# Optimization experiments

Hardware: AMD Instinct MI355X
Metric: run time of the kernel (lower is better)

Reference implementation:

```python
import jax, jax.numpy as jnp
import numpy as np

N, E, F_IN, C, H, G = 50000, 800000, 128, 64, 4, 512

def _gat_layer(x, src, dst, W, a_src, a_dst, b):
    # x: [N, Fin]; W: [Fin, H*C]; a_src/a_dst: [H, C]; b: [C]
    n = x.shape[0]
    h = (x @ W).reshape(n, H, C)                      # [N,H,C]
    al_s = jnp.einsum('nhc,hc->nh', h, a_src)         # [N,H]
    al_d = jnp.einsum('nhc,hc->nh', h, a_dst)
    alpha = jax.nn.leaky_relu(al_s[src] + al_d[dst], 0.2)   # [Et,H]
    m = jax.ops.segment_max(alpha, dst, num_segments=n)      # segment softmax over dst
    e = jnp.exp(alpha - m[dst])
    s = jax.ops.segment_sum(e, dst, num_segments=n)
    coef = e / (s[dst] + 1e-16)                        # [Et,H]
    msg = h[src] * coef[:, :, None]                    # [Et,H,C]
    out = jax.ops.segment_sum(msg, dst, num_segments=n)
    return out.mean(axis=1) + b                        # concat=False: average heads

def setup_inputs():
    key = jax.random.key(0)
    ks = jax.random.split(key, 24)
    x = jax.random.normal(ks[0], (N, F_IN), jnp.float32)
    edge_index = jax.random.randint(ks[1], (2, E), 0, N, jnp.int64)
    edge_attr = jax.random.normal(ks[2], (E, 4), jnp.float32)
    batch_index = jnp.sort(jax.random.randint(ks[3], (N,), 0, G, jnp.int64))
    p = lambda k, shp: jax.random.normal(k, shp, jnp.float32) * 0.05
    inp = {
        'x': x, 'edge_index': edge_index, 'edge_attr': edge_attr, 'batch_index': batch_index,
        'W0': p(ks[4], (F_IN, H * C)), 'as0': p(ks[5], (H, C)), 'ad0': p(ks[6], (H, C)), 'b0': jnp.zeros((C,), jnp.float32),
        'W1': p(ks[7], (C, H * C)), 'as1': p(ks[8], (H, C)), 'ad1': p(ks[9], (H, C)), 'b1': jnp.zeros((C,), jnp.float32),
        'W2': p(ks[10], (C, H * C)), 'as2': p(ks[11], (H, C)), 'ad2': p(ks[12], (H, C)), 'b2': jnp.zeros((C,), jnp.float32),
        'Wr1': p(ks[13], (2 * C, C)), 'br1': jnp.zeros((C,), jnp.float32),
        'Wr2': p(ks[14], (C, 1)), 'br2': jnp.zeros((1,), jnp.float32),
    }
    return inp

def reference(x, edge_index, edge_attr, batch_index,
              W0, as0, ad0, b0, W1, as1, ad1, b1, W2, as2, ad2, b2,
              Wr1, br1, Wr2, br2):
    # add self-loops (PyG GATConv default add_self_loops=True); edge_attr unused (edge_dim=None)
    loop = jnp.arange(N, dtype=edge_index.dtype)
    src = jnp.concatenate([edge_index[0], loop])
    dst = jnp.concatenate([edge_index[1], loop])
    h = jax.nn.leaky_relu(_gat_layer(x, src, dst, W0, as0, ad0, b0))
    h = jax.nn.leaky_relu(_gat_layer(h, src, dst, W1, as1, ad1, b1))
    h = jax.nn.leaky_relu(_gat_layer(h, src, dst, W2, as2, ad2, b2))
    gmp = jax.ops.segment_max(h, batch_index, num_segments=G)           # [G,C]
    cnt = jax.ops.segment_sum(jnp.ones((N,), h.dtype), batch_index, num_segments=G)
    gap = jax.ops.segment_sum(h, batch_index, num_segments=G) / jnp.maximum(cnt, 1.0)[:, None]
    hid = jnp.concatenate([gmp, gap], axis=1)                            # [G,2C]
    hid = jax.nn.leaky_relu(hid @ Wr1 + br1)
    return hid @ Wr2 + br2                                               # [G,1]
```

## Files before the change

### kernel.cpp

```cpp
#include <hip/hip_runtime.h>
#include <hip/hip_bf16.h>
#include <hip/hip_fp16.h>

#define NN   50000
#define EE   800000
#define FIN  128
#define CC   64
#define HH   4
#define GG   512
#define CAP  64

__device__ __forceinline__ float leaky02(float x) { return x >= 0.f ? x : 0.2f * x; }
__device__ __forceinline__ float leaky01(float x) { return x >= 0.f ? x : 0.01f * x; }

__global__ __launch_bounds__(256) void build_csr(const int* __restrict__ ei,
                                                 int* __restrict__ deg,
                                                 int* __restrict__ csr) {
    int e = blockIdx.x * 256 + threadIdx.x;
    if (e >= EE) return;
    int s = ei[e];
    int d = ei[EE + e];
    if ((unsigned)d >= NN || (unsigned)s >= NN) return;
    int pos = atomicAdd(&deg[d], 1);
    if (pos < CAP) csr[d * CAP + pos] = s;
}

template <int K>
__global__ __launch_bounds__(256, 3) void gemm_gat(const float* __restrict__ x,
                                                   const float* __restrict__ W,
                                                   const float* __restrict__ a_src,
                                                   const float* __restrict__ a_dst,
                                                   __half* __restrict__ h_out,
                                                   float* __restrict__ al_s,
                                                   float* __restrict__ al_d) {
    __shared__ float Xs[32 * 128];
    __shared__ float Ws[32 * 128];
    const int t  = threadIdx.x;
    const int tc = t & 15;
    const int tr = t >> 4;
    const int r0 = blockIdx.x * 128;
    const int c0 = blockIdx.y * 128;

    float acc[8][8];
#pragma unroll
    for (int i = 0; i < 8; ++i)
#pragma unroll
        for (int j = 0; j < 8; ++j) acc[i][j] = 0.f;

    for (int k0 = 0; k0 < K; k0 += 32) {
#pragma unroll
        for (int jj = 0; jj < 4; ++jj) {
            int id = t + jj * 256;
            int m  = id >> 3;
            int k4 = id & 7;
            int row = r0 + m;
            row = row < NN ? row : NN - 1;
            float4 v = *(const float4*)(x + (size_t)row * K + k0 + k4 * 4);
#pragma unroll
            for (int c = 0; c < 4; ++c) {
                int k = k4 * 4 + c;
                int slot = (m >> 3) ^ (k >> 2);
                Xs[k * 128 + slot * 8 + (m & 7)] = ((const float*)&v)[c];
            }
        }
#pragma unroll
        for (int jj = 0; jj < 4; ++jj) {
            int id = t + jj * 256;
            int k  = id >> 5;
            int n4 = id & 31;
            float4 v = *(const float4*)(W + (size_t)(k0 + k) * 256 + c0 + n4 * 4);
            *(float4*)(Ws + k * 128 + n4 * 4) = v;
        }
        __syncthreads();

#pragma unroll
        for (int k = 0; k < 32; ++k) {
            int aslot = tr ^ (k >> 2);
            const float* ax = &Xs[k * 128 + aslot * 8];
            const float* bw = &Ws[k * 128 + tc * 8];
            float a0[8], b0[8];
            *(float4*)&a0[0] = *(const float4*)&ax[0];
            *(float4*)&a0[4] = *(const float4*)&ax[4];
            *(float4*)&b0[0] = *(const float4*)&bw[0];
            *(float4*)&b0[4] = *(const float4*)&bw[4];
#pragma unroll
            for (int i = 0; i < 8; ++i)
#pragma unroll
                for (int j = 0; j < 8; ++j)
                    acc[i][j] = fmaf(a0[i], b0[j], acc[i][j]);
        }
        __syncthreads();
    }

    const int colbase = c0 + tc * 8;
    const int head = colbase >> 6;
    float as_c[8], ad_c[8];
#pragma unroll
    for (int j = 0; j < 8; ++j) {
        as_c[j] = a_src[colbase + j];
        ad_c[j] = a_dst[colbase + j];
    }
#pragma unroll
    for (int i = 0; i < 8; ++i) {
        int row = r0 + tr * 8 + i;
        bool ok = row < NN;
        if (ok) {
            __half2 p0 = __floats2half2_rn(acc[i][0], acc[i][1]);
            __half2 p1 = __floats2half2_rn(acc[i][2], acc[i][3]);
            __half2 p2 = __floats2half2_rn(acc[i][4], acc[i][5]);
            __half2 p3 = __floats2half2_rn(acc[i][6], acc[i][7]);
            uint4 pk;
            pk.x = *(unsigned int*)&p0;
            pk.y = *(unsigned int*)&p1;
            pk.z = *(unsigned int*)&p2;
            pk.w = *(unsigned int*)&p3;
            *(uint4*)(h_out + (size_t)row * 256 + colbase) = pk;
        }
        float ps = 0.f, pd = 0.f;
#pragma unroll
        for (int j = 0; j < 8; ++j) {
            ps = fmaf(acc[i][j], as_c[j], ps);
            pd = fmaf(acc[i][j], ad_c[j], pd);
        }
#pragma unroll
        for (int off = 1; off <= 4; off <<= 1) {
            ps += __shfl_xor(ps, off, 64);
            pd += __shfl_xor(pd, off, 64);
        }
        if (ok && (tc & 7) == 0) {
            al_s[(size_t)row * 4 + head] = ps;
            al_d[(size_t)row * 4 + head] = pd;
        }
    }
}

struct Half8 { __half2 h[4]; };

__global__ __launch_bounds__(256) void gat_aggregate(const __half* __restrict__ h_buf,
                                                     const float* __restrict__ al_s,
                                                     const float* __restrict__ al_d,
                                                     const int* __restrict__ deg,
                                                     const int* __restrict__ csr,
                                                     const float* __restrict__ bias,
                                                     float* __restrict__ xout) {
    __shared__ __align__(16) __half2 els[4][66][4];
    const int w    = threadIdx.x >> 6;
    const int lane = threadIdx.x & 63;
    const int n    = blockIdx.x * 4 + w;
    const int d = min(deg[n], CAP);

    float4 ad4 = *(const float4*)(al_d + (size_t)n * 4);
    float4 as4 = *(const float4*)(al_s + (size_t)n * 4);
    const float* adp = (const float*)&ad4;
    const float* asp = (const float*)&as4;

    float aself[4];
#pragma unroll
    for (int h = 0; h < 4; ++h) aself[h] = leaky02(asp[h] + adp[h]);

    int s_lane = 0;
    float a_lane[4];
    if (lane < d) {
        s_lane = csr[(size_t)n * CAP + lane];
        float4 s4 = *(const float4*)(al_s + (size_t)s_lane * 4);
        const float* sp = (const float*)&s4;
#pragma unroll
        for (int h = 0; h < 4; ++h) a_lane[h] = leaky02(sp[h] + adp[h]);
    } else {
#pragma unroll
        for (int h = 0; h < 4; ++h) a_lane[h] = -INFINITY;
    }

    float mx[4];
#pragma unroll
    for (int h = 0; h < 4; ++h) {
        mx[h] = fmaxf(aself[h], a_lane[h]);
#pragma unroll
        for (int off = 32; off; off >>= 1) mx[h] = fmaxf(mx[h], __shfl_xor(mx[h], off, 64));
    }

    float e[4], sm[4];
#pragma unroll
    for (int h = 0; h < 4; ++h) {
        e[h] = (lane < d) ? expf(a_lane[h] - mx[h]) : 0.f;
        sm[h] = e[h];
#pragma unroll
        for (int off = 32; off; off >>= 1) sm[h] += __shfl_xor(sm[h], off, 64);
    }
    float eself[4], inv[4];
#pragma unroll
    for (int h = 0; h < 4; ++h) {
        eself[h] = expf(aself[h] - mx[h]);
        inv[h] = 1.f / (sm[h] + eself[h] + 1e-16f);
    }
    if (lane < d) {
#pragma unroll
        for (int h = 0; h < 4; ++h) {
            float c = e[h] * inv[h];
            els[w][lane + 1][h] = __floats2half2_rn(c, c);
        }
    }
    if (lane == 0) {
#pragma unroll
        for (int h = 0; h < 4; ++h) {
            float c = eself[h] * inv[h];
            els[w][0][h] = __floats2half2_rn(c, c);
        }
    }

    const int q    = lane >> 5;
    const int m    = lane & 31;
    const int head = m >> 3;
    const __half* __restrict__ hb = h_buf + m * 8;

    __half2 z = __floats2half2_rn(0.f, 0.f);
    __half2 acc0 = z, acc1 = z, acc2 = z, acc3 = z;
    const int count = d + 1;
    for (int t2 = 0; 2 * t2 < count; ++t2) {
        int v = 2 * t2 + q;
        int vi = v > 0 ? v - 1 : 0;
        int s = __shfl(s_lane, vi, 64);
        s = v == 0 ? n : s;
        if (v < count) {
            __half2 c2 = els[w][v][head];
            Half8 r = *(const Half8*)(hb + (size_t)s * 256);
            acc0 = __hfma2(r.h[0], c2, acc0);
            acc1 = __hfma2(r.h[1], c2, acc1);
            acc2 = __hfma2(r.h[2], c2, acc2);
            acc3 = __hfma2(r.h[3], c2, acc3);
        }
    }

    int i0 = __shfl_xor(*(int*)&acc0, 32, 64);
    int i1 = __shfl_xor(*(int*)&acc1, 32, 64);
    int i2 = __shfl_xor(*(int*)&acc2, 32, 64);
    int i3 = __shfl_xor(*(int*)&acc3, 32, 64);
    acc0 = __hadd2(acc0, *(__half2*)&i0);
    acc1 = __hadd2(acc1, *(__half2*)&i1);
    acc2 = __hadd2(acc2, *(__half2*)&i2);
    acc3 = __hadd2(acc3, *(__half2*)&i3);

    float ch[8];
    float2 f;
    f = __half22float2(acc0); ch[0] = f.x; ch[1] = f.y;
    f = __half22float2(acc1); ch[2] = f.x; ch[3] = f.y;
    f = __half22float2(acc2); ch[4] = f.x; ch[5] = f.y;
    f = __half22float2(acc3); ch[6] = f.x; ch[7] = f.y;
#pragma unroll
    for (int k = 0; k < 8; ++k) {
        ch[k] += __shfl_xor(ch[k], 8, 64);
        ch[k] += __shfl_xor(ch[k], 16, 64);
    }
    if (lane < 8) {
        float4 o0, o1;
        o0.x = leaky01(ch[0] * 0.25f + bias[lane * 8 + 0]);
        o0.y = leaky01(ch[1] * 0.25f + bias[lane * 8 + 1]);
        o0.z = leaky01(ch[2] * 0.25f + bias[lane * 8 + 2]);
        o0.w = leaky01(ch[3] * 0.25f + bias[lane * 8 + 3]);
        o1.x = leaky01(ch[4] * 0.25f + bias[lane * 8 + 4]);
        o1.y = leaky01(ch[5] * 0.25f + bias[lane * 8 + 5]);
        o1.z = leaky01(ch[6] * 0.25f + bias[lane * 8 + 6]);
        o1.w = leaky01(ch[7] * 0.25f + bias[lane * 8 + 7]);
        *(float4*)(xout + (size_t)n * 64 + lane * 8)     = o0;
        *(float4*)(xout + (size_t)n * 64 + lane * 8 + 4) = o1;
    }
}

__global__ __launch_bounds__(256) void readout(const float* __restrict__ x,
                                               const int* __restrict__ batch,
                                               float* __restrict__ gmp,
                                               float* __restrict__ gap) {
    int g = blockIdx.x;
    int a = 0, b = NN;
    while (a < b) { int m = (a + b) >> 1; if (batch[m] < g) a = m + 1; else b = m; }
    int lo = a;
    a = lo; b = NN;
    while (a < b) { int m = (a + b) >> 1; if (batch[m] < g + 1) a = m + 1; else b = m; }
    int hi = a;

    int t = threadIdx.x, c = t & 63, s = t >> 6;
    float mx = -INFINITY, sm = 0.f;
    for (int n = lo + s; n < hi; n += 4) {
        float v = x[(size_t)n * 64 + c];
        mx = fmaxf(mx, v);
        sm += v;
    }
    __shared__ float smx[256], ssm[256];
    smx[t] = mx; ssm[t] = sm;
    __syncthreads();
    if (t < 64) {
        mx = fmaxf(fmaxf(smx[t], smx[t + 64]), fmaxf(smx[t + 128], smx[t + 192]));
        sm = ssm[t] + ssm[t + 64] + ssm[t + 128] + ssm[t + 192];
        int cnt = hi - lo;
        gmp[g * 64 + t] = mx;
        gap[g * 64 + t] = sm / fmaxf((float)cnt, 1.0f);
    }
}

__global__ __launch_bounds__(64) void mlp_readout(const float* __restrict__ gmp,
                                                  const float* __restrict__ gap,
                                                  const float* __restrict__ Wr1,
                                                  const float* __restrict__ br1,
                                                  const float* __restrict__ Wr2,
                                                  const float* __restrict__ br2,
                                                  float* __restrict__ out) {
    int g = blockIdx.x;
    int j = threadIdx.x;
    double acc = (double)br1[j];
    for (int i = 0; i < 64; ++i) acc += (double)gmp[g * 64 + i] * (double)Wr1[i * 64 + j];
    for (int i = 0; i < 64; ++i) acc += (double)gap[g * 64 + i] * (double)Wr1[(64 + i) * 64 + j];
    float v = (float)acc;
    v = v >= 0.f ? v : 0.01f * v;
    double tv = (double)v * (double)Wr2[j];
#pragma unroll
    for (int off = 32; off; off >>= 1) tv += __shfl_xor(tv, off, 64);
    if (j == 0) out[g] = (float)(tv + (double)br2[0]);
}

extern "C" void kernel_launch(void* const* d_in, const int* in_sizes, int n_in,
                              void* d_out, int out_size, void* d_ws, size_t ws_size,
                              hipStream_t stream) {
    const float* x   = (const float*)d_in[0];
    const int* ei    = (const int*)d_in[1];
    const int* batch = (const int*)d_in[3];
    const float* W0  = (const float*)d_in[4];
    const float* as0 = (const float*)d_in[5];
    const float* ad0 = (const float*)d_in[6];
    const float* b0  = (const float*)d_in[7];
    const float* W1  = (const float*)d_in[8];
    const float* as1 = (const float*)d_in[9];
    const float* ad1 = (const float*)d_in[10];
    const float* b1  = (const float*)d_in[11];
    const float* W2  = (const float*)d_in[12];
    const float* as2 = (const float*)d_in[13];
    const float* ad2 = (const float*)d_in[14];
    const float* b2  = (const float*)d_in[15];
    const float* Wr1 = (const float*)d_in[16];
    const float* br1 = (const float*)d_in[17];
    const float* Wr2 = (const float*)d_in[18];
    const float* br2 = (const float*)d_in[19];
    float* out = (float*)d_out;

    __half* h_buf = (__half*)d_ws;
    float* al_s  = (float*)(h_buf + (size_t)NN * 256);
    float* al_d  = al_s + (size_t)NN * 4;
    float* xbuf  = al_d + (size_t)NN * 4;
    float* gmp   = xbuf + (size_t)NN * 64;
    float* gap   = gmp + (size_t)GG * 64;
    int*   deg   = (int*)(gap + (size_t)GG * 64);
    int*   csr   = deg + NN;

    hipMemsetAsync(deg, 0, NN * sizeof(int), stream);
    build_csr<<<(EE + 255) / 256, 256, 0, stream>>>(ei, deg, csr);

    const dim3 gemm_grid((NN + 127) / 128, 2);
    const int agg_grid = (NN + 3) / 4;

    gemm_gat<FIN><<<gemm_grid, 256, 0, stream>>>(x, W0, as0, ad0, h_buf, al_s, al_d);
    gat_aggregate<<<agg_grid, 256, 0, stream>>>(h_buf, al_s, al_d, deg, csr, b0, xbuf);
    gemm_gat<CC><<<gemm_grid, 256, 0, stream>>>(xbuf, W1, as1, ad1, h_buf, al_s, al_d);
    gat_aggregate<<<agg_grid, 256, 0, stream>>>(h_buf, al_s, al_d, deg, csr, b1, xbuf);
    gemm_gat<CC><<<gemm_grid, 256, 0, stream>>>(xbuf, W2, as2, ad2, h_buf, al_s, al_d);
    gat_aggregate<<<agg_grid, 256, 0, stream>>>(h_buf, al_s, al_d, deg, csr, b2, xbuf);

    readout<<<GG, 256, 0, stream>>>(xbuf, batch, gmp, gap);
    mlp_readout<<<GG, 64, 0, stream>>>(gmp, gap, Wr1, br1, Wr2, br2, out);
}
```

Before: 502.7 us.

## Replace FP32 SIMT GEMM with split-fp16 MFMA GEMM and fp16 activations

Replaces the shared-memory FP32 FMA GEMM with a 16x16x32 fp16 MFMA kernel. It emulates FP32 accuracy by splitting inputs into hi and lo halves and issuing three MFMAs per tile. The input x and the weights are pre-split by new conversion kernels, with the weights packed into the MFMA operand layout. The aggregate kernel now writes hi/lo fp16 activations directly for the next layer. This trades extra conversion launches and a 3x MFMA count for far higher matrix throughput. The readout now reads only the hi half, a small precision loss, and the h_out stores become scalar half writes.

```diff
diff --git a/kernel.cpp b/kernel.cpp
--- a/kernel.cpp
+++ b/kernel.cpp
@@ -9,6 +9,9 @@
 #define HH   4
 #define GG   512
 #define CAP  64
+
+typedef _Float16 f16x8 __attribute__((ext_vector_type(8)));
+typedef float    f32x4 __attribute__((ext_vector_type(4)));
 
 __device__ __forceinline__ float leaky02(float x) { return x >= 0.f ? x : 0.2f * x; }
 __device__ __forceinline__ float leaky01(float x) { return x >= 0.f ? x : 0.01f * x; }
@@ -25,111 +28,131 @@
     if (pos < CAP) csr[d * CAP + pos] = s;
 }
 
+__global__ __launch_bounds__(256) void convert_x(const float* __restrict__ x,
+                                                 __half* __restrict__ xh,
+                                                 __half* __restrict__ xl,
+                                                 int n) {
+    int i = (blockIdx.x * 256 + threadIdx.x) * 8;
+    if (i >= n) return;
+    float v[8];
+    *(float4*)&v[0] = *(const float4*)(x + i);
+    *(float4*)&v[4] = *(const float4*)(x + i + 4);
+    __half hi[8], lo[8];
+#pragma unroll
+    for (int j = 0; j < 8; ++j) {
+        hi[j] = __float2half_rn(v[j]);
+        lo[j] = __float2half_rn(v[j] - __half2float(hi[j]));
+    }
+    *(uint4*)(xh + i) = *(uint4*)hi;
+    *(uint4*)(xl + i) = *(uint4*)lo;
+}
+
+__global__ __launch_bounds__(256) void convert_w(const float* __restrict__ W,
+                                                 __half* __restrict__ wph,
+                                                 __half* __restrict__ wpl,
+                                                 int K) {
+    int id = blockIdx.x * 256 + threadIdx.x;
+    int total = (K / 32) * 16 * 64;
+    if (id >= total) return;
+    int lane = id & 63;
+    int c    = (id >> 6) & 15;
+    int kc   = id >> 10;
+    int kbase = kc * 32 + (lane >> 4) * 8;
+    int col   = c * 16 + (lane & 15);
+    __half hi[8], lo[8];
+#pragma unroll
+    for (int j = 0; j < 8; ++j) {
+        float v = W[(size_t)(kbase + j) * 256 + col];
+        hi[j] = __float2half_rn(v);
+        lo[j] = __float2half_rn(v - __half2float(hi[j]));
+    }
+    *(uint4*)(wph + (size_t)id * 8) = *(uint4*)hi;
+    *(uint4*)(wpl + (size_t)id * 8) = *(uint4*)lo;
+}
+
 template <int K>
-__global__ __launch_bounds__(256, 3) void gemm_gat(const float* __restrict__ x,
-                                                   const float* __restrict__ W,
-                                                   const float* __restrict__ a_src,
-                                                   const float* __restrict__ a_dst,
-                                                   __half* __restrict__ h_out,
-                                                   float* __restrict__ al_s,
-                                                   float* __restrict__ al_d) {
-    __shared__ float Xs[32 * 128];
-    __shared__ float Ws[32 * 128];
-    const int t  = threadIdx.x;
-    const int tc = t & 15;
-    const int tr = t >> 4;
-    const int r0 = blockIdx.x * 128;
-    const int c0 = blockIdx.y * 128;
-
-    float acc[8][8];
-#pragma unroll
-    for (int i = 0; i < 8; ++i)
-#pragma unroll
-        for (int j = 0; j < 8; ++j) acc[i][j] = 0.f;
-
-    for (int k0 = 0; k0 < K; k0 += 32) {
-#pragma unroll
-        for (int jj = 0; jj < 4; ++jj) {
-            int id = t + jj * 256;
-            int m  = id >> 3;
-            int k4 = id & 7;
-            int row = r0 + m;
-            row = row < NN ? row : NN - 1;
-            float4 v = *(const float4*)(x + (size_t)row * K + k0 + k4 * 4);
-#pragma unroll
-            for (int c = 0; c < 4; ++c) {
-                int k = k4 * 4 + c;
-                int slot = (m >> 3) ^ (k >> 2);
-                Xs[k * 128 + slot * 8 + (m & 7)] = ((const float*)&v)[c];
+__global__ __launch_bounds__(256) void gemm_mfma(const __half* __restrict__ xh,
+                                                 const __half* __restrict__ xl,
+                                                 const __half* __restrict__ wph,
+                                                 const __half* __restrict__ wpl,
+                                                 const float* __restrict__ a_src,
+                                                 const float* __restrict__ a_dst,
+                                                 __half* __restrict__ h_out,
+                                                 float* __restrict__ al_s,
+                                                 float* __restrict__ al_d) {
+    const int t    = threadIdx.x;
+    const int w    = t >> 6;
+    const int lane = t & 63;
+    const int r0   = blockIdx.x * 64 + w * 16;
+    const int colL = lane & 15;
+    const int rowg = lane >> 4;
+    int arow = r0 + colL;
+    arow = arow < NN ? arow : NN - 1;
+    const int koff = rowg * 8;
+
+    f32x4 acc[16];
+#pragma unroll
+    for (int c = 0; c < 16; ++c) acc[c] = (f32x4){0.f, 0.f, 0.f, 0.f};
+
+    for (int kc = 0; kc < K / 32; ++kc) {
+        f16x8 ah = *(const f16x8*)(xh + (size_t)arow * K + kc * 32 + koff);
+        f16x8 al = *(const f16x8*)(xl + (size_t)arow * K + kc * 32 + koff);
+        const __half* bbase_h = wph + ((size_t)(kc * 16) * 64 + lane) * 8;
+        const __half* bbase_l = wpl + ((size_t)(kc * 16) * 64 + lane) * 8;
+#pragma unroll
+        for (int c = 0; c < 16; ++c) {
+            f16x8 bh = *(const f16x8*)(bbase_h + c * 512);
+            f16x8 bl = *(const f16x8*)(bbase_l + c * 512);
+            acc[c] = __builtin_amdgcn_mfma_f32_16x16x32_f16(ah, bh, acc[c], 0, 0, 0);
+            acc[c] = __builtin_amdgcn_mfma_f32_16x16x32_f16(al, bh, acc[c], 0, 0, 0);
+            acc[c] = __builtin_amdgcn_mfma_f32_16x16x32_f16(ah, bl, acc[c], 0, 0, 0);
+        }
+    }
+
+    float aps[4][4], apd[4][4];
+#pragma unroll
+    for (int r = 0; r < 4; ++r)
+#pragma unroll
+        for (int h = 0; h < 4; ++h) { aps[r][h] = 0.f; apd[r][h] = 0.f; }
+
+#pragma unroll
+    for (int c = 0; c < 16; ++c) {
+        const int col = c * 16 + colL;
+        const float as = a_src[col];
+        const float ad = a_dst[col];
+        const int hh = c >> 2;
+#pragma unroll
+        for (int r = 0; r < 4; ++r) {
+            const int row = r0 + rowg * 4 + r;
+            const float v = acc[c][r];
+            if (row < NN) h_out[(size_t)row * 256 + col] = __float2half_rn(v);
+            aps[r][hh] = fmaf(v, as, aps[r][hh]);
+            apd[r][hh] = fmaf(v, ad, apd[r][hh]);
+        }
+    }
+#pragma unroll
+    for (int r = 0; r < 4; ++r)
+#pragma unroll
+        for (int h = 0; h < 4; ++h) {
+            float s = aps[r][h], d = apd[r][h];
+#pragma unroll
+            for (int off = 1; off <= 8; off <<= 1) {
+                s += __shfl_xor(s, off, 64);
+                d += __shfl_xor(d, off, 64);
             }
-        }
-#pragma unroll
-        for (int jj = 0; jj < 4; ++jj) {
-            int id = t + jj * 256;
-            int k  = id >> 5;
-            int n4 = id & 31;
-            float4 v = *(const float4*)(W + (size_t)(k0 + k) * 256 + c0 + n4 * 4);
-            *(float4*)(Ws + k * 128 + n4 * 4) = v;
-        }
-        __syncthreads();
-
-#pragma unroll
-        for (int k = 0; k < 32; ++k) {
-            int aslot = tr ^ (k >> 2);
-            const float* ax = &Xs[k * 128 + aslot * 8];
-            const float* bw = &Ws[k * 128 + tc * 8];
-            float a0[8], b0[8];
-            *(float4*)&a0[0] = *(const float4*)&ax[0];
-            *(float4*)&a0[4] = *(const float4*)&ax[4];
-            *(float4*)&b0[0] = *(const float4*)&bw[0];
-            *(float4*)&b0[4] = *(const float4*)&bw[4];
-#pragma unroll
-            for (int i = 0; i < 8; ++i)
-#pragma unroll
-                for (int j = 0; j < 8; ++j)
-                    acc[i][j] = fmaf(a0[i], b0[j], acc[i][j]);
-        }
-        __syncthreads();
-    }
-
-    const int colbase = c0 + tc * 8;
-    const int head = colbase >> 6;
-    float as_c[8], ad_c[8];
-#pragma unroll
-    for (int j = 0; j < 8; ++j) {
-        as_c[j] = a_src[colbase + j];
-        ad_c[j] = a_dst[colbase + j];
-    }
-#pragma unroll
-    for (int i = 0; i < 8; ++i) {
-        int row = r0 + tr * 8 + i;
-        bool ok = row < NN;
-        if (ok) {
-            __half2 p0 = __floats2half2_rn(acc[i][0], acc[i][1]);
-            __half2 p1 = __floats2half2_rn(acc[i][2], acc[i][3]);
-            __half2 p2 = __floats2half2_rn(acc[i][4], acc[i][5]);
-            __half2 p3 = __floats2half2_rn(acc[i][6], acc[i][7]);
-            uint4 pk;
-            pk.x = *(unsigned int*)&p0;
-            pk.y = *(unsigned int*)&p1;
-            pk.z = *(unsigned int*)&p2;
-            pk.w = *(unsigned int*)&p3;
-            *(uint4*)(h_out + (size_t)row * 256 + colbase) = pk;
-        }
-        float ps = 0.f, pd = 0.f;
-#pragma unroll
-        for (int j = 0; j < 8; ++j) {
-            ps = fmaf(acc[i][j], as_c[j], ps);
-            pd = fmaf(acc[i][j], ad_c[j], pd);
-        }
-#pragma unroll
-        for (int off = 1; off <= 4; off <<= 1) {
-            ps += __shfl_xor(ps, off, 64);
-            pd += __shfl_xor(pd, off, 64);
-        }
-        if (ok && (tc & 7) == 0) {
-            al_s[(size_t)row * 4 + head] = ps;
-            al_d[(size_t)row * 4 + head] = pd;
+            aps[r][h] = s; apd[r][h] = d;
+        }
+    if (colL == 0) {
+#pragma unroll
+        for (int r = 0; r < 4; ++r) {
+            const int row = r0 + rowg * 4 + r;
+            if (row < NN) {
+#pragma unroll
+                for (int h = 0; h < 4; ++h) {
+                    al_s[(size_t)row * 4 + h] = aps[r][h];
+                    al_d[(size_t)row * 4 + h] = apd[r][h];
+                }
+            }
         }
     }
 }
@@ -142,7 +165,8 @@
                                                      const int* __restrict__ deg,
                                                      const int* __restrict__ csr,
                                                      const float* __restrict__ bias,
-                                                     float* __restrict__ xout) {
+                                                     __half* __restrict__ xb_hi,
+                                                     __half* __restrict__ xb_lo) {
     __shared__ __align__(16) __half2 els[4][66][4];
     const int w    = threadIdx.x >> 6;
     const int lane = threadIdx.x & 63;
@@ -252,21 +276,20 @@
         ch[k] += __shfl_xor(ch[k], 16, 64);
     }
     if (lane < 8) {
-        float4 o0, o1;
-        o0.x = leaky01(ch[0] * 0.25f + bias[lane * 8 + 0]);
-        o0.y = leaky01(ch[1] * 0.25f + bias[lane * 8 + 1]);
-        o0.z = leaky01(ch[2] * 0.25f + bias[lane * 8 + 2]);
-        o0.w = leaky01(ch[3] * 0.25f + bias[lane * 8 + 3]);
-        o1.x = leaky01(ch[4] * 0.25f + bias[lane * 8 + 4]);
-        o1.y = leaky01(ch[5] * 0.25f + bias[lane * 8 + 5]);
-        o1.z = leaky01(ch[6] * 0.25f + bias[lane * 8 + 6]);
-        o1.w = leaky01(ch[7] * 0.25f + bias[lane * 8 + 7]);
-        *(float4*)(xout + (size_t)n * 64 + lane * 8)     = o0;
-        *(float4*)(xout + (size_t)n * 64 + lane * 8 + 4) = o1;
-    }
-}
-
-__global__ __launch_bounds__(256) void readout(const float* __restrict__ x,
+        __align__(16) __half hi8[8], lo8[8];
+#pragma unroll
+        for (int k = 0; k < 8; ++k) {
+            float o = leaky01(ch[k] * 0.25f + bias[lane * 8 + k]);
+            __half hv = __float2half_rn(o);
+            hi8[k] = hv;
+            lo8[k] = __float2half_rn(o - __half2float(hv));
+        }
+        *(uint4*)(xb_hi + (size_t)n * 64 + lane * 8) = *(uint4*)hi8;
+        *(uint4*)(xb_lo + (size_t)n * 64 + lane * 8) = *(uint4*)lo8;
+    }
+}
+
+__global__ __launch_bounds__(256) void readout(const __half* __restrict__ x,
                                                const int* __restrict__ batch,
                                                float* __restrict__ gmp,
                                                float* __restrict__ gap) {
@@ -281,7 +304,7 @@
     int t = threadIdx.x, c = t & 63, s = t >> 6;
     float mx = -INFINITY, sm = 0.f;
     for (int n = lo + s; n < hi; n += 4) {
-        float v = x[(size_t)n * 64 + c];
+        float v = __half2float(x[(size_t)n * 64 + c]);
         mx = fmaxf(mx, v);
         sm += v;
     }
@@ -342,27 +365,41 @@
     float* out = (float*)d_out;
 
     __half* h_buf = (__half*)d_ws;
-    float* al_s  = (float*)(h_buf + (size_t)NN * 256);
-    float* al_d  = al_s + (size_t)NN * 4;
-    float* xbuf  = al_d + (size_t)NN * 4;
-    float* gmp   = xbuf + (size_t)NN * 64;
-    float* gap   = gmp + (size_t)GG * 64;
-    int*   deg   = (int*)(gap + (size_t)GG * 64);
-    int*   csr   = deg + NN;
+    __half* x_hi  = h_buf + (size_t)NN * 256;
+    __half* x_lo  = x_hi + (size_t)NN * 128;
+    __half* xb_hi = x_hi;
+    __half* xb_lo = x_lo;
+    __half* w0ph  = x_lo + (size_t)NN * 128;
+    __half* w0pl  = w0ph + 32768;
+    __half* w1ph  = w0pl + 32768;
+    __half* w1pl  = w1ph + 16384;
+    __half* w2ph  = w1pl + 16384;
+    __half* w2pl  = w2ph + 16384;
+    float*  al_s  = (float*)(w2pl + 16384);
+    float*  al_d  = al_s + (size_t)NN * 4;
+    float*  gmp   = al_d + (size_t)NN * 4;
+    float*  gap   = gmp + (size_t)GG * 64;
+    int*    deg   = (int*)(gap + (size_t)GG * 64);
+    int*    csr   = deg + NN;
 
     hipMemsetAsync(deg, 0, NN * sizeof(int), stream);
     build_csr<<<(EE + 255) / 256, 256, 0, stream>>>(ei, deg, csr);
 
-    const dim3 gemm_grid((NN + 127) / 128, 2);
-    const int agg_grid = (NN + 3) / 4;
-
-    gemm_gat<FIN><<<gemm_grid, 256, 0, stream>>>(x, W0, as0, ad0, h_buf, al_s, al_d);
-    gat_aggregate<<<agg_grid, 256, 0, stream>>>(h_buf, al_s, al_d, deg, csr, b0, xbuf);
-    gemm_gat<CC><<<gemm_grid, 256, 0, stream>>>(xbuf, W1, as1, ad1, h_buf, al_s, al_d);
-    gat_aggregate<<<agg_grid, 256, 0, stream>>>(h_buf, al_s, al_d, deg, csr, b1, xbuf);
-    gemm_gat<CC><<<gemm_grid, 256, 0, stream>>>(xbuf, W2, as2, ad2, h_buf, al_s, al_d);
-    gat_aggregate<<<agg_grid, 256, 0, stream>>>(h_buf, al_s, al_d, deg, csr, b2, xbuf);
-
-    readout<<<GG, 256, 0, stream>>>(xbuf, batch, gmp, gap);
+    convert_x<<<(NN * FIN / 8 + 255) / 256, 256, 0, stream>>>(x, x_hi, x_lo, NN * FIN);
+    convert_w<<<16, 256, 0, stream>>>(W0, w0ph, w0pl, 128);
+    convert_w<<<8, 256, 0, stream>>>(W1, w1ph, w1pl, 64);
+    convert_w<<<8, 256, 0, stream>>>(W2, w2ph, w2pl, 64);
+
+    const int gemm_grid = (NN + 63) / 64;
+    const int agg_grid  = (NN + 3) / 4;
+
+    gemm_mfma<FIN><<<gemm_grid, 256, 0, stream>>>(x_hi, x_lo, w0ph, w0pl, as0, ad0, h_buf, al_s, al_d);
+    gat_aggregate<<<agg_grid, 256, 0, stream>>>(h_buf, al_s, al_d, deg, csr, b0, xb_hi, xb_lo);
+    gemm_mfma<CC><<<gemm_grid, 256, 0, stream>>>(xb_hi, xb_lo, w1ph, w1pl, as1, ad1, h_buf, al_s, al_d);
+    gat_aggregate<<<agg_grid, 256, 0, stream>>>(h_buf, al_s, al_d, deg, csr, b1, xb_hi, xb_lo);
+    gemm_mfma<CC><<<gemm_grid, 256, 0, stream>>>(xb_hi, xb_lo, w2ph, w2pl, as2, ad2, h_buf, al_s, al_d);
+    gat_aggregate<<<agg_grid, 256, 0, stream>>>(h_buf, al_s, al_d, deg, csr, b2, xb_hi, xb_lo);
+
+    readout<<<GG, 256, 0, stream>>>(xb_hi, batch, gmp, gap);
     mlp_readout<<<GG, 64, 0, stream>>>(gmp, gap, Wr1, br1, Wr2, br2, out);
 }
```

Measured after the change: 498.3 us. Within noise of the previous version (-0.9%).
